# Performance work log

Measured on AMD Instinct MI355X. Metric: run time of the kernel, lower is better.

Reference implementation:

```python
import jax, jax.numpy as jnp
import numpy as np
import math

B, S, D_MODEL, H = 2, 2048, 2048, 16
HD = D_MODEL // H  # head_dim = 128


def setup_inputs() -> dict:
    key = jax.random.key(0)
    ks = jax.random.split(key, 10)
    x = jax.random.normal(ks[0], (B, S, D_MODEL), dtype=jnp.float32)
    # RoPE tables: interleaved-pair layout matching rotate_half (adjacent dims form pairs)
    inv_freq = 1.0 / (10000.0 ** (jnp.arange(0, HD, 2, dtype=jnp.float32) / HD))  # [HD/2]
    angles = jnp.arange(S, dtype=jnp.float32)[:, None] * inv_freq[None, :]        # [S, HD/2]
    angles = jnp.repeat(angles, 2, axis=-1)                                       # [S, HD]
    cos, sin = jnp.cos(angles), jnp.sin(angles)
    # causal mask (1 = keep), broadcastable to [B,H,S,S]
    attn_mask = jnp.tril(jnp.ones((S, S), dtype=bool))[None, None]
    scale = 1.0 / math.sqrt(D_MODEL)
    Wq = jax.random.normal(ks[1], (D_MODEL, D_MODEL), dtype=jnp.float32) * scale
    Wk = jax.random.normal(ks[2], (D_MODEL, D_MODEL), dtype=jnp.float32) * scale
    Wv = jax.random.normal(ks[3], (D_MODEL, D_MODEL), dtype=jnp.float32) * scale
    Wo = jax.random.normal(ks[4], (D_MODEL, D_MODEL), dtype=jnp.float32) * scale
    bq = jnp.zeros((D_MODEL,), jnp.float32)
    bk = jnp.zeros((D_MODEL,), jnp.float32)
    bv = jnp.zeros((D_MODEL,), jnp.float32)
    bo = jnp.zeros((D_MODEL,), jnp.float32)
    return {"x": x, "cos": cos, "sin": sin, "attn_mask": attn_mask,
            "Wq": Wq, "bq": bq, "Wk": Wk, "bk": bk, "Wv": Wv, "bv": bv, "Wo": Wo, "bo": bo}


def _rotate_half(x):
    # pairs adjacent dims: (x0,x1) -> (-x1,x0)
    xr = x.reshape(*x.shape[:-1], -1, 2)
    x1, x2 = xr[..., 0], xr[..., 1]
    return jnp.stack([-x2, x1], axis=-1).reshape(x.shape)


def reference(x, cos, sin, attn_mask, Wq, bq, Wk, bk, Wv, bv, Wo, bo):
    b, s, _ = x.shape
    q = (x @ Wq.T + bq).reshape(b, s, H, HD).transpose(0, 2, 1, 3)  # [B,H,S,HD]
    k = (x @ Wk.T + bk).reshape(b, s, H, HD).transpose(0, 2, 1, 3)
    v = (x @ Wv.T + bv).reshape(b, s, H, HD).transpose(0, 2, 1, 3)
    c = cos[None, None]  # [1,1,S,HD]
    sn = sin[None, None]
    q = q * c + _rotate_half(q) * sn
    k = k * c + _rotate_half(k) * sn
    scores = jnp.einsum('bhqd,bhkd->bhqk', q, k) / math.sqrt(HD)  # [B,H,S,S]
    scores = jnp.where(attn_mask, scores, -jnp.inf)
    attn = jax.nn.softmax(scores, axis=-1)
    out = jnp.einsum('bhqk,bhkd->bhqd', attn, v)  # [B,H,S,HD]
    out = out.transpose(0, 2, 1, 3).reshape(b, s, H * HD)
    return out @ Wo.T + bo
```

## Files before the change

kernel.cpp:

```cpp
#include <hip/hip_runtime.h>
#include <math.h>

typedef __attribute__((ext_vector_type(8))) __bf16 bf16x8;
typedef __attribute__((ext_vector_type(4))) float f32x4;
typedef __attribute__((ext_vector_type(4))) unsigned short us4;
typedef unsigned short u16;
typedef unsigned int u32;

#define DEVI static __device__ __forceinline__

DEVI u16 f2bf(float f) {
  union { float f; unsigned u; } v; v.f = f;
  unsigned r = v.u + 0x7fffu + ((v.u >> 16) & 1u);
  return (u16)(r >> 16);
}

DEVI void async16(const void* g, void* l) {
  __builtin_amdgcn_global_load_lds((const __attribute__((address_space(1))) void*)g,
                                   (__attribute__((address_space(3))) void*)l, 16, 0, 0);
}

DEVI u32 pkbf(float lo, float hi) {
  u32 r;
  asm("v_cvt_pk_bf16_f32 %0, %1, %2" : "=v"(r) : "v"(lo), "v"(hi));
  return r;
}

__global__ __launch_bounds__(256) void cast_bf16(const float* __restrict__ in,
                                                 u16* __restrict__ out, int n) {
  int i = (blockIdx.x * 256 + threadIdx.x) * 4;
  if (i >= n) return;
  float4 v = *(const float4*)(in + i);
  us4 o = { f2bf(v.x), f2bf(v.y), f2bf(v.z), f2bf(v.w) };
  *(us4*)(out + i) = o;
}

template<int MODE>
__global__ __launch_bounds__(256, 2)
void gemm_bt(const u16* __restrict__ A, const u16* __restrict__ B,
             const float* __restrict__ bias,
             const float* __restrict__ cosT, const float* __restrict__ sinT,
             void* __restrict__ outp)
{
  __shared__ __align__(16) u16 As[4096];
  __shared__ __align__(16) u16 Bs[4096];
  const int t = threadIdx.x, w = t >> 6, lane = t & 63;
  const int lrow = lane & 15, lk8 = (lane >> 4) * 8;
  const int brow = blockIdx.y * 128, bcol = blockIdx.x * 128;
  const int wr = (w >> 1) * 64, wc = (w & 1) * 64;

  f32x4 acc[4][4] = {};

  for (int k0 = 0; k0 < 2048; k0 += 32) {
#pragma unroll
    for (int r = 0; r < 2; ++r) {
      int e = (r * 256 + t) * 8;
      async16(A + (size_t)(brow + (e >> 5)) * 2048 + k0 + (e & 31), As + r * 2048 + w * 512);
      async16(B + (size_t)(bcol + (e >> 5)) * 2048 + k0 + (e & 31), Bs + r * 2048 + w * 512);
    }
    __syncthreads();
    bf16x8 a[4], b[4];
#pragma unroll
    for (int m = 0; m < 4; ++m) a[m] = *(const bf16x8*)(As + (wr + m * 16 + lrow) * 32 + lk8);
#pragma unroll
    for (int n = 0; n < 4; ++n) b[n] = *(const bf16x8*)(Bs + (wc + n * 16 + lrow) * 32 + lk8);
#pragma unroll
    for (int m = 0; m < 4; ++m)
#pragma unroll
      for (int n = 0; n < 4; ++n)
        acc[m][n] = __builtin_amdgcn_mfma_f32_16x16x32_bf16(a[m], b[n], acc[m][n], 0, 0, 0);
    __syncthreads();
  }

#pragma unroll
  for (int mi = 0; mi < 4; ++mi) {
#pragma unroll
    for (int ni = 0; ni < 4; ++ni) {
      f32x4 v = acc[mi][ni];
      const int row0 = brow + wr + mi * 16 + (lane >> 4) * 4;
      const int col = bcol + wc + ni * 16 + lrow;
      if constexpr (MODE == 3) {
        float* O = (float*)outp;
        const float bv = bias[col];
#pragma unroll
        for (int r = 0; r < 4; ++r)
          O[(size_t)(row0 + r) * 2048 + col] = v[r] + bv;
      } else if constexpr (MODE == 0 || MODE == 1) {
        u16* O = (u16*)outp;
        const float bv = bias[col];
        const int h = col >> 7, d = col & 127;
        const float sgn = (d & 1) ? 1.f : -1.f;
        const float QSCL = 0.08838834764831845f * 1.44269504088896340f;
#pragma unroll
        for (int r = 0; r < 4; ++r) {
          const int row = row0 + r, bb = row >> 11, s = row & 2047;
          float q = v[r] + bv;
          float p = __shfl_xor(q, 1);
          float o = q * cosT[s * 128 + d] + sgn * p * sinT[s * 128 + d];
          if constexpr (MODE == 0) o *= QSCL;
          u16* base = O + ((size_t)(bb * 16 + h) * 2048 + s) * 128;
          if constexpr (MODE == 0) {
            base[d] = f2bf(o);
          } else {
            *(u16*)((char*)base + (((unsigned)(d << 1)) ^ (unsigned)((s & 7) << 4))) = f2bf(o);
          }
        }
      } else {
        u16* O = (u16*)outp;
        const float bv = bias[col];
        const int h = col >> 7, d = col & 127;
        const int bb = row0 >> 11, s = row0 & 2047;
        us4 ov;
#pragma unroll
        for (int r = 0; r < 4; ++r) ov[r] = f2bf(v[r] + bv);
        const int l = s & 63;
        const int kt = l >> 4, g2 = (l >> 2) & 3;
        const int c = ((kt >> 1) << 5) + (g2 << 3) + ((kt & 1) << 2);
        u16* base = O + ((size_t)(bb * 16 + h) * 128 + d) * 2048 + (s & ~63);
        *(us4*)((char*)base + ((unsigned)(c << 1) ^ (unsigned)((d & 7) << 4))) = ov;
      }
    }
  }
}

__global__ __launch_bounds__(256, 2)
void attn_fwd(const u16* __restrict__ Q, const u16* __restrict__ K,
              const u16* __restrict__ Vt, u16* __restrict__ AO)
{
  __shared__ __align__(16) u16 Ks[2][64 * 128];
  __shared__ __align__(16) u16 Vs[2][128 * 64];
  const int t = threadIdx.x, w = t >> 6, lane = t & 63;
  const int lrow = lane & 15, g = lane >> 4, lk8 = g * 8;
  const int id = blockIdx.x;
  const int bh = (id & 7) | (((id >> 3) & 3) << 3);
  const int pr = id >> 5;
  const u16* Qg = Q + (size_t)bh * 2048 * 128;
  const u16* Kg = K + (size_t)bh * 2048 * 128;
  const u16* Vg = Vt + (size_t)bh * 128 * 2048;
  const int bb = bh >> 4, h = bh & 15;

  for (int half = 0; half < 2; ++half) {
    const int qt = half ? (31 - pr) : pr;
    const int q0 = qt * 64, qw = q0 + w * 16;
    const int nkv = qt + 1;
    const int qg = qw + lrow;

    bf16x8 qf[4];
#pragma unroll
    for (int c = 0; c < 4; ++c)
      qf[c] = *(const bf16x8*)(Qg + (size_t)(qw + lrow) * 128 + lk8 + c * 32);

    f32x4 acc_o[8] = {};
    float m = -1e30f, lsum = 0.f;

    auto stage = [&](int i, int b) {
#pragma unroll
      for (int r = 0; r < 4; ++r) {
        int e = (r * 256 + t) * 8;
        async16(Kg + (size_t)i * 8192 + e, &Ks[b][r * 2048 + w * 512]);
        async16(Vg + (size_t)(e >> 6) * 2048 + i * 64 + (e & 63), &Vs[b][r * 2048 + w * 512]);
      }
    };

    stage(0, 0);
    for (int i = 0; i < nkv; ++i) {
      const int cur = i & 1;
      const bool pfch = (i + 1) < nkv;
      if (pfch) stage(i + 1, cur ^ 1);
      if (pfch) asm volatile("s_waitcnt vmcnt(8)" ::: "memory");
      else      asm volatile("s_waitcnt vmcnt(0)" ::: "memory");
      __builtin_amdgcn_s_barrier();
      __builtin_amdgcn_sched_barrier(0);

      f32x4 sc[4];
      __builtin_amdgcn_s_setprio(1);
#pragma unroll
      for (int kt = 0; kt < 4; ++kt) {
        f32x4 s = {};
        const int krow = kt * 16 + lrow;
        const char* kbase = (const char*)(&Ks[cur][krow * 128]);
        const unsigned sw = (unsigned)((krow & 7) << 4);
#pragma unroll
        for (int c = 0; c < 4; ++c) {
          bf16x8 kf = *(const bf16x8*)(kbase + ((unsigned)((lk8 + c * 32) << 1) ^ sw));
          s = __builtin_amdgcn_mfma_f32_16x16x32_bf16(kf, qf[c], s, 0, 0, 0);
        }
        sc[kt] = s;
      }
      __builtin_amdgcn_s_setprio(0);

      float p[4][4];
      const bool lastblk = (i == qt);
      if (lastblk) {
#pragma unroll
        for (int kt = 0; kt < 4; ++kt)
#pragma unroll
          for (int r = 0; r < 4; ++r) {
            int kg = i * 64 + kt * 16 + g * 4 + r;
            p[kt][r] = (kg > qg) ? -1e30f : sc[kt][r];
          }
      } else {
#pragma unroll
        for (int kt = 0; kt < 4; ++kt)
#pragma unroll
          for (int r = 0; r < 4; ++r) p[kt][r] = sc[kt][r];
      }

      float mm = p[0][0];
#pragma unroll
      for (int kt = 0; kt < 4; ++kt)
#pragma unroll
        for (int r = 0; r < 4; ++r) mm = fmaxf(mm, p[kt][r]);
      mm = fmaxf(mm, __shfl_xor(mm, 16));
      mm = fmaxf(mm, __shfl_xor(mm, 32));

      float rs = 0.f;
      if (__any(mm > m + 8.f)) {
        const float mn = fmaxf(m, mm);
        const float corr = exp2f(m - mn);
        m = mn;
#pragma unroll
        for (int kt = 0; kt < 4; ++kt)
#pragma unroll
          for (int r = 0; r < 4; ++r) { p[kt][r] = exp2f(p[kt][r] - m); rs += p[kt][r]; }
        rs += __shfl_xor(rs, 16);
        rs += __shfl_xor(rs, 32);
        lsum = lsum * corr + rs;
#pragma unroll
        for (int nt = 0; nt < 8; ++nt)
#pragma unroll
          for (int r = 0; r < 4; ++r) acc_o[nt][r] *= corr;
      } else {
#pragma unroll
        for (int kt = 0; kt < 4; ++kt)
#pragma unroll
          for (int r = 0; r < 4; ++r) { p[kt][r] = exp2f(p[kt][r] - m); rs += p[kt][r]; }
        rs += __shfl_xor(rs, 16);
        rs += __shfl_xor(rs, 32);
        lsum += rs;
      }

      bf16x8 pb[2];
#pragma unroll
      for (int kc = 0; kc < 2; ++kc) {
        union { u32 d[4]; bf16x8 v; } u;
        u.d[0] = pkbf(p[2 * kc][0], p[2 * kc][1]);
        u.d[1] = pkbf(p[2 * kc][2], p[2 * kc][3]);
        u.d[2] = pkbf(p[2 * kc + 1][0], p[2 * kc + 1][1]);
        u.d[3] = pkbf(p[2 * kc + 1][2], p[2 * kc + 1][3]);
        pb[kc] = u.v;
      }

      __builtin_amdgcn_s_setprio(1);
#pragma unroll
      for (int nt = 0; nt < 8; ++nt) {
        const int vrow = nt * 16 + lrow;
        const char* vbase = (const char*)(&Vs[cur][vrow * 64]);
        const unsigned sw2 = (unsigned)((vrow & 7) << 4);
#pragma unroll
        for (int kc = 0; kc < 2; ++kc) {
          bf16x8 vf = *(const bf16x8*)(vbase + ((unsigned)((lk8 + kc * 32) << 1) ^ sw2));
          acc_o[nt] = __builtin_amdgcn_mfma_f32_16x16x32_bf16(vf, pb[kc], acc_o[nt], 0, 0, 0);
        }
      }
      __builtin_amdgcn_s_setprio(0);
      __builtin_amdgcn_s_barrier();
    }

    const float inv_l = 1.f / lsum;
#pragma unroll
    for (int nt = 0; nt < 8; ++nt) {
      us4 ov;
#pragma unroll
      for (int r = 0; r < 4; ++r) ov[r] = f2bf(acc_o[nt][r] * inv_l);
      *(us4*)(AO + ((size_t)(bb * 2048 + qg)) * 2048 + h * 128 + nt * 16 + g * 4) = ov;
    }
  }
}

extern "C" void kernel_launch(void* const* d_in, const int* in_sizes, int n_in,
                              void* d_out, int out_size, void* d_ws, size_t ws_size,
                              hipStream_t stream) {
  const float* x    = (const float*)d_in[0];
  const float* cosT = (const float*)d_in[1];
  const float* sinT = (const float*)d_in[2];
  const float* Wq   = (const float*)d_in[4];
  const float* bq   = (const float*)d_in[5];
  const float* Wk   = (const float*)d_in[6];
  const float* bk   = (const float*)d_in[7];
  const float* Wv   = (const float*)d_in[8];
  const float* bv   = (const float*)d_in[9];
  const float* Wo   = (const float*)d_in[10];
  const float* bo   = (const float*)d_in[11];
  float* out = (float*)d_out;

  char* ws = (char*)d_ws;
  u16* xb  = (u16*)(ws);
  u16* Wqb = (u16*)(ws + (16u << 20));
  u16* Wkb = (u16*)(ws + (24u << 20));
  u16* Wvb = (u16*)(ws + (32u << 20));
  u16* Wob = (u16*)(ws + (40u << 20));
  u16* Qb  = (u16*)(ws + (48u << 20));
  u16* Kb  = (u16*)(ws + (64u << 20));
  u16* Vtb = (u16*)(ws + (80u << 20));
  u16* AOb = (u16*)(ws + (96u << 20));

  cast_bf16<<<8192, 256, 0, stream>>>(x,  xb,  4096 * 2048);
  cast_bf16<<<4096, 256, 0, stream>>>(Wq, Wqb, 2048 * 2048);
  cast_bf16<<<4096, 256, 0, stream>>>(Wk, Wkb, 2048 * 2048);
  cast_bf16<<<4096, 256, 0, stream>>>(Wv, Wvb, 2048 * 2048);
  cast_bf16<<<4096, 256, 0, stream>>>(Wo, Wob, 2048 * 2048);

  dim3 gg(16, 32);
  gemm_bt<0><<<gg, 256, 0, stream>>>(xb, Wqb, bq, cosT, sinT, (void*)Qb);
  gemm_bt<1><<<gg, 256, 0, stream>>>(xb, Wkb, bk, cosT, sinT, (void*)Kb);
  gemm_bt<2><<<gg, 256, 0, stream>>>(xb, Wvb, bv, nullptr, nullptr, (void*)Vtb);

  attn_fwd<<<512, 256, 0, stream>>>(Qb, Kb, Vtb, AOb);

  gemm_bt<3><<<gg, 256, 0, stream>>>(AOb, Wob, bo, nullptr, nullptr, (void*)out);
}
```

Before: 289.0 us.

## Replace GEMMs with fused QKV triple-buffered 8-wave 256x128 tile kernel

Replaces the simple single-buffered 128x128 GEMM with a 512-thread, 256x128-tile kernel that uses a 64-wide K step, a triple-buffered LDS ring of async global-to-LDS loads, XOR-swizzled LDS layout and ping-pong MFMA phases with priority hints. The Q, K and V projections are merged into one launch with a combined grid selecting the weight slab per tile. The output projection uses the same kernel. The aim is to hide global memory latency, avoid LDS bank conflicts, cut barrier overhead per MFMA and remove two launches. The cost is more complex synchronisation that relies on hand-written vmcnt waits and about 144KB of LDS per block.

```diff
diff --git a/kernel.cpp b/kernel.cpp
--- a/kernel.cpp
+++ b/kernel.cpp
@@ -35,80 +35,132 @@
   *(us4*)(out + i) = o;
 }
 
-template<int MODE>
-__global__ __launch_bounds__(256, 2)
-void gemm_bt(const u16* __restrict__ A, const u16* __restrict__ B,
-             const float* __restrict__ bias,
-             const float* __restrict__ cosT, const float* __restrict__ sinT,
-             void* __restrict__ outp)
+__global__ __launch_bounds__(512, 2)
+void gemm8p(const u16* __restrict__ A,
+            const u16* __restrict__ W0, const u16* __restrict__ W1, const u16* __restrict__ W2,
+            const float* __restrict__ biasQ, const float* __restrict__ biasK,
+            const float* __restrict__ biasV,
+            const float* __restrict__ cosT, const float* __restrict__ sinT,
+            void* __restrict__ out0, void* __restrict__ out1, void* __restrict__ out2,
+            int ntn, int qkv)
 {
-  __shared__ __align__(16) u16 As[4096];
-  __shared__ __align__(16) u16 Bs[4096];
+  __shared__ __align__(16) char lds[3 * 49152];
   const int t = threadIdx.x, w = t >> 6, lane = t & 63;
-  const int lrow = lane & 15, lk8 = (lane >> 4) * 8;
-  const int brow = blockIdx.y * 128, bcol = blockIdx.x * 128;
-  const int wr = (w >> 1) * 64, wc = (w & 1) * 64;
+  const int lrow = lane & 15, g = lane >> 4, lk8 = g * 8;
+  const int nt = blockIdx.x % ntn, mt = blockIdx.x / ntn;
+  const int slab = qkv ? (nt >> 4) : 3;
+  const u16* Bp = (slab == 1) ? W1 : (slab == 2) ? W2 : W0;
+  const int brow = mt * 256;
+  const int bcol = (qkv ? (nt & 15) : nt) * 128;
+  const int wm = w >> 1, wn = w & 1;
+
+  size_t soff[6];
+#pragma unroll
+  for (int j = 0; j < 6; ++j) {
+    int p = j * 8192 + t * 16;
+    int pr = (j < 4) ? p : (p - 32768);
+    int r = pr >> 7;
+    int c = ((pr ^ ((r & 7) << 4)) & 127) >> 1;
+    soff[j] = (j < 4) ? ((size_t)(brow + r) * 2048 + c)
+                      : ((size_t)(bcol + r) * 2048 + c);
+  }
+  auto stage = [&](int tile, int j, char* buf) {
+    const u16* src = (j < 4) ? A : Bp;
+    async16(src + soff[j] + tile * 64, buf + j * 8192 + t * 16);
+  };
+
+  int offA[4][2], offB[4][2];
+#pragma unroll
+  for (int m = 0; m < 4; ++m)
+#pragma unroll
+    for (int kk = 0; kk < 2; ++kk) {
+      const int c = (lk8 + kk * 32) * 2;
+      const int ra = wm * 64 + m * 16 + lrow;
+      offA[m][kk] = (ra * 128 + c) ^ ((ra & 7) << 4);
+      const int rb = wn * 64 + m * 16 + lrow;
+      offB[m][kk] = 32768 + ((rb * 128 + c) ^ ((rb & 7) << 4));
+    }
 
   f32x4 acc[4][4] = {};
 
-  for (int k0 = 0; k0 < 2048; k0 += 32) {
-#pragma unroll
-    for (int r = 0; r < 2; ++r) {
-      int e = (r * 256 + t) * 8;
-      async16(A + (size_t)(brow + (e >> 5)) * 2048 + k0 + (e & 31), As + r * 2048 + w * 512);
-      async16(B + (size_t)(bcol + (e >> 5)) * 2048 + k0 + (e & 31), Bs + r * 2048 + w * 512);
-    }
-    __syncthreads();
-    bf16x8 a[4], b[4];
-#pragma unroll
-    for (int m = 0; m < 4; ++m) a[m] = *(const bf16x8*)(As + (wr + m * 16 + lrow) * 32 + lk8);
-#pragma unroll
-    for (int n = 0; n < 4; ++n) b[n] = *(const bf16x8*)(Bs + (wc + n * 16 + lrow) * 32 + lk8);
-#pragma unroll
-    for (int m = 0; m < 4; ++m)
+#pragma unroll
+  for (int j = 0; j < 6; ++j) stage(0, j, lds);
+#pragma unroll
+  for (int j = 0; j < 6; ++j) stage(1, j, lds + 49152);
+  asm volatile("s_waitcnt vmcnt(6)" ::: "memory");
+  __builtin_amdgcn_s_barrier();
+
+  for (int tt = 0; tt < 32; ++tt) {
+    char* cur = lds + (tt % 3) * 49152;
+    char* nxt = lds + ((tt + 2) % 3) * 49152;
+    const bool st = (tt + 2) < 32;
+
+    bf16x8 bfr[4][2], afr[2][2];
+#pragma unroll
+    for (int n = 0; n < 4; ++n)
+#pragma unroll
+      for (int kk = 0; kk < 2; ++kk) bfr[n][kk] = *(const bf16x8*)(cur + offB[n][kk]);
+#pragma unroll
+    for (int m = 0; m < 2; ++m)
+#pragma unroll
+      for (int kk = 0; kk < 2; ++kk) afr[m][kk] = *(const bf16x8*)(cur + offA[m][kk]);
+    if (st) { stage(tt + 2, 0, nxt); stage(tt + 2, 1, nxt); stage(tt + 2, 2, nxt); }
+    __builtin_amdgcn_s_barrier();
+    asm volatile("s_waitcnt lgkmcnt(0)" ::: "memory");
+    __builtin_amdgcn_sched_barrier(0);
+    __builtin_amdgcn_s_setprio(1);
+#pragma unroll
+    for (int m = 0; m < 2; ++m)
 #pragma unroll
       for (int n = 0; n < 4; ++n)
-        acc[m][n] = __builtin_amdgcn_mfma_f32_16x16x32_bf16(a[m], b[n], acc[m][n], 0, 0, 0);
-    __syncthreads();
+#pragma unroll
+        for (int kk = 0; kk < 2; ++kk)
+          acc[m][n] = __builtin_amdgcn_mfma_f32_16x16x32_bf16(afr[m][kk], bfr[n][kk], acc[m][n], 0, 0, 0);
+    __builtin_amdgcn_s_setprio(0);
+    __builtin_amdgcn_s_barrier();
+
+#pragma unroll
+    for (int m = 0; m < 2; ++m)
+#pragma unroll
+      for (int kk = 0; kk < 2; ++kk) afr[m][kk] = *(const bf16x8*)(cur + offA[m + 2][kk]);
+    if (st) { stage(tt + 2, 3, nxt); stage(tt + 2, 4, nxt); stage(tt + 2, 5, nxt); }
+    if (tt < 31) {
+      if (st) asm volatile("s_waitcnt vmcnt(6)" ::: "memory");
+      else    asm volatile("s_waitcnt vmcnt(0)" ::: "memory");
+    }
+    __builtin_amdgcn_s_barrier();
+    asm volatile("s_waitcnt lgkmcnt(0)" ::: "memory");
+    __builtin_amdgcn_sched_barrier(0);
+    __builtin_amdgcn_s_setprio(1);
+#pragma unroll
+    for (int m = 0; m < 2; ++m)
+#pragma unroll
+      for (int n = 0; n < 4; ++n)
+#pragma unroll
+        for (int kk = 0; kk < 2; ++kk)
+          acc[m + 2][n] = __builtin_amdgcn_mfma_f32_16x16x32_bf16(afr[m][kk], bfr[n][kk], acc[m + 2][n], 0, 0, 0);
+    __builtin_amdgcn_s_setprio(0);
+    __builtin_amdgcn_s_barrier();
   }
 
+  const int g4 = g * 4;
 #pragma unroll
   for (int mi = 0; mi < 4; ++mi) {
 #pragma unroll
     for (int ni = 0; ni < 4; ++ni) {
       f32x4 v = acc[mi][ni];
-      const int row0 = brow + wr + mi * 16 + (lane >> 4) * 4;
-      const int col = bcol + wc + ni * 16 + lrow;
-      if constexpr (MODE == 3) {
-        float* O = (float*)outp;
-        const float bv = bias[col];
+      const int row0 = brow + wm * 64 + mi * 16 + g4;
+      const int cols = bcol + wn * 64 + ni * 16 + lrow;
+      if (slab == 3) {
+        float* O = (float*)out0;
+        const float bv = biasQ[cols];
 #pragma unroll
         for (int r = 0; r < 4; ++r)
-          O[(size_t)(row0 + r) * 2048 + col] = v[r] + bv;
-      } else if constexpr (MODE == 0 || MODE == 1) {
-        u16* O = (u16*)outp;
-        const float bv = bias[col];
-        const int h = col >> 7, d = col & 127;
-        const float sgn = (d & 1) ? 1.f : -1.f;
-        const float QSCL = 0.08838834764831845f * 1.44269504088896340f;
-#pragma unroll
-        for (int r = 0; r < 4; ++r) {
-          const int row = row0 + r, bb = row >> 11, s = row & 2047;
-          float q = v[r] + bv;
-          float p = __shfl_xor(q, 1);
-          float o = q * cosT[s * 128 + d] + sgn * p * sinT[s * 128 + d];
-          if constexpr (MODE == 0) o *= QSCL;
-          u16* base = O + ((size_t)(bb * 16 + h) * 2048 + s) * 128;
-          if constexpr (MODE == 0) {
-            base[d] = f2bf(o);
-          } else {
-            *(u16*)((char*)base + (((unsigned)(d << 1)) ^ (unsigned)((s & 7) << 4))) = f2bf(o);
-          }
-        }
-      } else {
-        u16* O = (u16*)outp;
-        const float bv = bias[col];
-        const int h = col >> 7, d = col & 127;
+          O[(size_t)(row0 + r) * 2048 + cols] = v[r] + bv;
+      } else if (slab == 2) {
+        u16* O = (u16*)out2;
+        const float bv = biasV[cols];
+        const int h = cols >> 7, d = cols & 127;
         const int bb = row0 >> 11, s = row0 & 2047;
         us4 ov;
 #pragma unroll
@@ -118,6 +170,25 @@
         const int c = ((kt >> 1) << 5) + (g2 << 3) + ((kt & 1) << 2);
         u16* base = O + ((size_t)(bb * 16 + h) * 128 + d) * 2048 + (s & ~63);
         *(us4*)((char*)base + ((unsigned)(c << 1) ^ (unsigned)((d & 7) << 4))) = ov;
+      } else {
+        u16* O = (u16*)(slab ? out1 : out0);
+        const float bv = slab ? biasK[cols] : biasQ[cols];
+        const int h = cols >> 7, d = cols & 127;
+        const float sgn = (d & 1) ? 1.f : -1.f;
+        const float QSCL = 0.08838834764831845f * 1.44269504088896340f;
+#pragma unroll
+        for (int r = 0; r < 4; ++r) {
+          const int row = row0 + r, bb = row >> 11, s = row & 2047;
+          float q = v[r] + bv;
+          float p = __shfl_xor(q, 1);
+          float o = q * cosT[s * 128 + d] + sgn * p * sinT[s * 128 + d];
+          u16* base = O + ((size_t)(bb * 16 + h) * 2048 + s) * 128;
+          if (slab == 0) {
+            base[d] = f2bf(o * QSCL);
+          } else {
+            *(u16*)((char*)base + (((unsigned)(d << 1)) ^ (unsigned)((s & 7) << 4))) = f2bf(o);
+          }
+        }
       }
     }
   }
@@ -311,12 +382,11 @@
   cast_bf16<<<4096, 256, 0, stream>>>(Wv, Wvb, 2048 * 2048);
   cast_bf16<<<4096, 256, 0, stream>>>(Wo, Wob, 2048 * 2048);
 
-  dim3 gg(16, 32);
-  gemm_bt<0><<<gg, 256, 0, stream>>>(xb, Wqb, bq, cosT, sinT, (void*)Qb);
-  gemm_bt<1><<<gg, 256, 0, stream>>>(xb, Wkb, bk, cosT, sinT, (void*)Kb);
-  gemm_bt<2><<<gg, 256, 0, stream>>>(xb, Wvb, bv, nullptr, nullptr, (void*)Vtb);
+  gemm8p<<<768, 512, 0, stream>>>(xb, Wqb, Wkb, Wvb, bq, bk, bv, cosT, sinT,
+                                  (void*)Qb, (void*)Kb, (void*)Vtb, 48, 1);
 
   attn_fwd<<<512, 256, 0, stream>>>(Qb, Kb, Vtb, AOb);
 
-  gemm_bt<3><<<gg, 256, 0, stream>>>(AOb, Wob, bo, nullptr, nullptr, (void*)out);
-}
+  gemm8p<<<256, 512, 0, stream>>>(AOb, Wob, Wob, Wob, bo, bo, bo, nullptr, nullptr,
+                                  (void*)out, nullptr, nullptr, 16, 0);
+}
```

New measurement: 274.7 us. 5.0% less time.

## Merge QKV projections into one launch and double query rows per attention wave

Applied to the files above, without the earlier changes.

The Q, K and V projection GEMMs now run as a single launch with a 48-wide grid, where each block picks its weight slab and epilogue at runtime. The output projection uses the same kernel with the slab forced to the plain fp32 path, and the GEMM launch bound is raised to 4 blocks per CU. The attention kernel now has each wave handle two 16-row query sub-tiles (128 query rows per block), so every K/V tile loaded into LDS is reused twice, and the grid is halved to 256 blocks. The costs are more registers per wave in attention, fewer blocks for load balancing, and runtime branching in the GEMM epilogue.

```diff
diff --git a/kernel.cpp b/kernel.cpp
--- a/kernel.cpp
+++ b/kernel.cpp
@@ -35,18 +35,22 @@
   *(us4*)(out + i) = o;
 }
 
-template<int MODE>
-__global__ __launch_bounds__(256, 2)
-void gemm_bt(const u16* __restrict__ A, const u16* __restrict__ B,
-             const float* __restrict__ bias,
+__global__ __launch_bounds__(256, 4)
+void gemm128(const u16* __restrict__ A,
+             const u16* __restrict__ W0, const u16* __restrict__ W1, const u16* __restrict__ W2,
+             const float* __restrict__ biasQ, const float* __restrict__ biasK,
+             const float* __restrict__ biasV,
              const float* __restrict__ cosT, const float* __restrict__ sinT,
-             void* __restrict__ outp)
+             void* __restrict__ out0, void* __restrict__ out1, void* __restrict__ out2,
+             int qkv)
 {
   __shared__ __align__(16) u16 As[4096];
   __shared__ __align__(16) u16 Bs[4096];
   const int t = threadIdx.x, w = t >> 6, lane = t & 63;
   const int lrow = lane & 15, lk8 = (lane >> 4) * 8;
-  const int brow = blockIdx.y * 128, bcol = blockIdx.x * 128;
+  const int slab = qkv ? (blockIdx.x >> 4) : 3;
+  const u16* Bp = (slab == 1) ? W1 : (slab == 2) ? W2 : W0;
+  const int brow = blockIdx.y * 128, bcol = (blockIdx.x & 15) * 128;
   const int wr = (w >> 1) * 64, wc = (w & 1) * 64;
 
   f32x4 acc[4][4] = {};
@@ -56,7 +60,7 @@
     for (int r = 0; r < 2; ++r) {
       int e = (r * 256 + t) * 8;
       async16(A + (size_t)(brow + (e >> 5)) * 2048 + k0 + (e & 31), As + r * 2048 + w * 512);
-      async16(B + (size_t)(bcol + (e >> 5)) * 2048 + k0 + (e & 31), Bs + r * 2048 + w * 512);
+      async16(Bp + (size_t)(bcol + (e >> 5)) * 2048 + k0 + (e & 31), Bs + r * 2048 + w * 512);
     }
     __syncthreads();
     bf16x8 a[4], b[4];
@@ -78,37 +82,17 @@
     for (int ni = 0; ni < 4; ++ni) {
       f32x4 v = acc[mi][ni];
       const int row0 = brow + wr + mi * 16 + (lane >> 4) * 4;
-      const int col = bcol + wc + ni * 16 + lrow;
-      if constexpr (MODE == 3) {
-        float* O = (float*)outp;
-        const float bv = bias[col];
+      const int cols = bcol + wc + ni * 16 + lrow;
+      if (slab == 3) {
+        float* O = (float*)out0;
+        const float bv = biasQ[cols];
 #pragma unroll
         for (int r = 0; r < 4; ++r)
-          O[(size_t)(row0 + r) * 2048 + col] = v[r] + bv;
-      } else if constexpr (MODE == 0 || MODE == 1) {
-        u16* O = (u16*)outp;
-        const float bv = bias[col];
-        const int h = col >> 7, d = col & 127;
-        const float sgn = (d & 1) ? 1.f : -1.f;
-        const float QSCL = 0.08838834764831845f * 1.44269504088896340f;
-#pragma unroll
-        for (int r = 0; r < 4; ++r) {
-          const int row = row0 + r, bb = row >> 11, s = row & 2047;
-          float q = v[r] + bv;
-          float p = __shfl_xor(q, 1);
-          float o = q * cosT[s * 128 + d] + sgn * p * sinT[s * 128 + d];
-          if constexpr (MODE == 0) o *= QSCL;
-          u16* base = O + ((size_t)(bb * 16 + h) * 2048 + s) * 128;
-          if constexpr (MODE == 0) {
-            base[d] = f2bf(o);
-          } else {
-            *(u16*)((char*)base + (((unsigned)(d << 1)) ^ (unsigned)((s & 7) << 4))) = f2bf(o);
-          }
-        }
-      } else {
-        u16* O = (u16*)outp;
-        const float bv = bias[col];
-        const int h = col >> 7, d = col & 127;
+          O[(size_t)(row0 + r) * 2048 + cols] = v[r] + bv;
+      } else if (slab == 2) {
+        u16* O = (u16*)out2;
+        const float bv = biasV[cols];
+        const int h = cols >> 7, d = cols & 127;
         const int bb = row0 >> 11, s = row0 & 2047;
         us4 ov;
 #pragma unroll
@@ -118,12 +102,31 @@
         const int c = ((kt >> 1) << 5) + (g2 << 3) + ((kt & 1) << 2);
         u16* base = O + ((size_t)(bb * 16 + h) * 128 + d) * 2048 + (s & ~63);
         *(us4*)((char*)base + ((unsigned)(c << 1) ^ (unsigned)((d & 7) << 4))) = ov;
+      } else {
+        u16* O = (u16*)(slab ? out1 : out0);
+        const float bv = slab ? biasK[cols] : biasQ[cols];
+        const int h = cols >> 7, d = cols & 127;
+        const float sgn = (d & 1) ? 1.f : -1.f;
+        const float QSCL = 0.08838834764831845f * 1.44269504088896340f;
+#pragma unroll
+        for (int r = 0; r < 4; ++r) {
+          const int row = row0 + r, bb = row >> 11, s = row & 2047;
+          float q = v[r] + bv;
+          float p = __shfl_xor(q, 1);
+          float o = q * cosT[s * 128 + d] + sgn * p * sinT[s * 128 + d];
+          u16* base = O + ((size_t)(bb * 16 + h) * 2048 + s) * 128;
+          if (slab == 0) {
+            base[d] = f2bf(o * QSCL);
+          } else {
+            *(u16*)((char*)base + (((unsigned)(d << 1)) ^ (unsigned)((s & 7) << 4))) = f2bf(o);
+          }
+        }
       }
     }
   }
 }
 
-__global__ __launch_bounds__(256, 2)
+__global__ __launch_bounds__(256)
 void attn_fwd(const u16* __restrict__ Q, const u16* __restrict__ K,
               const u16* __restrict__ Vt, u16* __restrict__ AO)
 {
@@ -132,35 +135,37 @@
   const int t = threadIdx.x, w = t >> 6, lane = t & 63;
   const int lrow = lane & 15, g = lane >> 4, lk8 = g * 8;
   const int id = blockIdx.x;
-  const int bh = (id & 7) | (((id >> 3) & 3) << 3);
+  const int bh = id & 31;
   const int pr = id >> 5;
   const u16* Qg = Q + (size_t)bh * 2048 * 128;
   const u16* Kg = K + (size_t)bh * 2048 * 128;
   const u16* Vg = Vt + (size_t)bh * 128 * 2048;
   const int bb = bh >> 4, h = bh & 15;
 
+  auto stage = [&](int i, int b) {
+#pragma unroll
+    for (int r = 0; r < 4; ++r) {
+      int e = (r * 256 + t) * 8;
+      async16(Kg + (size_t)i * 8192 + e, &Ks[b][r * 2048 + w * 512]);
+      async16(Vg + (size_t)(e >> 6) * 2048 + i * 64 + (e & 63), &Vs[b][r * 2048 + w * 512]);
+    }
+  };
+
   for (int half = 0; half < 2; ++half) {
-    const int qt = half ? (31 - pr) : pr;
-    const int q0 = qt * 64, qw = q0 + w * 16;
-    const int nkv = qt + 1;
-    const int qg = qw + lrow;
-
-    bf16x8 qf[4];
-#pragma unroll
-    for (int c = 0; c < 4; ++c)
-      qf[c] = *(const bf16x8*)(Qg + (size_t)(qw + lrow) * 128 + lk8 + c * 32);
-
-    f32x4 acc_o[8] = {};
-    float m = -1e30f, lsum = 0.f;
-
-    auto stage = [&](int i, int b) {
-#pragma unroll
-      for (int r = 0; r < 4; ++r) {
-        int e = (r * 256 + t) * 8;
-        async16(Kg + (size_t)i * 8192 + e, &Ks[b][r * 2048 + w * 512]);
-        async16(Vg + (size_t)(e >> 6) * 2048 + i * 64 + (e & 63), &Vs[b][r * 2048 + w * 512]);
-      }
-    };
+    const int qt = half ? (15 - pr) : pr;
+    const int qw = qt * 128 + w * 32;
+    const int nkv = 2 * (qt + 1);
+    const int qg0 = qw + lrow;
+
+    bf16x8 qf[2][4];
+#pragma unroll
+    for (int s2 = 0; s2 < 2; ++s2)
+#pragma unroll
+      for (int c = 0; c < 4; ++c)
+        qf[s2][c] = *(const bf16x8*)(Qg + (size_t)(qw + s2 * 16 + lrow) * 128 + lk8 + c * 32);
+
+    f32x4 acc[2][8] = {};
+    float m[2] = { -1e30f, -1e30f }, lsum[2] = { 0.f, 0.f };
 
     stage(0, 0);
     for (int i = 0; i < nkv; ++i) {
@@ -172,83 +177,88 @@
       __builtin_amdgcn_s_barrier();
       __builtin_amdgcn_sched_barrier(0);
 
-      f32x4 sc[4];
+      f32x4 sc[2][4];
       __builtin_amdgcn_s_setprio(1);
 #pragma unroll
       for (int kt = 0; kt < 4; ++kt) {
-        f32x4 s = {};
+        f32x4 s0 = {}, s1 = {};
         const int krow = kt * 16 + lrow;
         const char* kbase = (const char*)(&Ks[cur][krow * 128]);
         const unsigned sw = (unsigned)((krow & 7) << 4);
 #pragma unroll
         for (int c = 0; c < 4; ++c) {
           bf16x8 kf = *(const bf16x8*)(kbase + ((unsigned)((lk8 + c * 32) << 1) ^ sw));
-          s = __builtin_amdgcn_mfma_f32_16x16x32_bf16(kf, qf[c], s, 0, 0, 0);
-        }
-        sc[kt] = s;
+          s0 = __builtin_amdgcn_mfma_f32_16x16x32_bf16(kf, qf[0][c], s0, 0, 0, 0);
+          s1 = __builtin_amdgcn_mfma_f32_16x16x32_bf16(kf, qf[1][c], s1, 0, 0, 0);
+        }
+        sc[0][kt] = s0; sc[1][kt] = s1;
       }
       __builtin_amdgcn_s_setprio(0);
 
-      float p[4][4];
-      const bool lastblk = (i == qt);
-      if (lastblk) {
+      const bool guard = (i * 64 + 63) > qw;
+      bf16x8 pb[2][2];
+#pragma unroll
+      for (int s2 = 0; s2 < 2; ++s2) {
+        const int qgs = qg0 + s2 * 16;
+        float p[4][4];
+        if (guard) {
+#pragma unroll
+          for (int kt = 0; kt < 4; ++kt)
+#pragma unroll
+            for (int r = 0; r < 4; ++r) {
+              int kg = i * 64 + kt * 16 + g * 4 + r;
+              p[kt][r] = (kg > qgs) ? -1e30f : sc[s2][kt][r];
+            }
+        } else {
+#pragma unroll
+          for (int kt = 0; kt < 4; ++kt)
+#pragma unroll
+            for (int r = 0; r < 4; ++r) p[kt][r] = sc[s2][kt][r];
+        }
+
+        float mm = p[0][0];
 #pragma unroll
         for (int kt = 0; kt < 4; ++kt)
 #pragma unroll
-          for (int r = 0; r < 4; ++r) {
-            int kg = i * 64 + kt * 16 + g * 4 + r;
-            p[kt][r] = (kg > qg) ? -1e30f : sc[kt][r];
-          }
-      } else {
-#pragma unroll
-        for (int kt = 0; kt < 4; ++kt)
-#pragma unroll
-          for (int r = 0; r < 4; ++r) p[kt][r] = sc[kt][r];
-      }
-
-      float mm = p[0][0];
-#pragma unroll
-      for (int kt = 0; kt < 4; ++kt)
-#pragma unroll
-        for (int r = 0; r < 4; ++r) mm = fmaxf(mm, p[kt][r]);
-      mm = fmaxf(mm, __shfl_xor(mm, 16));
-      mm = fmaxf(mm, __shfl_xor(mm, 32));
-
-      float rs = 0.f;
-      if (__any(mm > m + 8.f)) {
-        const float mn = fmaxf(m, mm);
-        const float corr = exp2f(m - mn);
-        m = mn;
-#pragma unroll
-        for (int kt = 0; kt < 4; ++kt)
-#pragma unroll
-          for (int r = 0; r < 4; ++r) { p[kt][r] = exp2f(p[kt][r] - m); rs += p[kt][r]; }
-        rs += __shfl_xor(rs, 16);
-        rs += __shfl_xor(rs, 32);
-        lsum = lsum * corr + rs;
-#pragma unroll
-        for (int nt = 0; nt < 8; ++nt)
-#pragma unroll
-          for (int r = 0; r < 4; ++r) acc_o[nt][r] *= corr;
-      } else {
-#pragma unroll
-        for (int kt = 0; kt < 4; ++kt)
-#pragma unroll
-          for (int r = 0; r < 4; ++r) { p[kt][r] = exp2f(p[kt][r] - m); rs += p[kt][r]; }
-        rs += __shfl_xor(rs, 16);
-        rs += __shfl_xor(rs, 32);
-        lsum += rs;
-      }
-
-      bf16x8 pb[2];
-#pragma unroll
-      for (int kc = 0; kc < 2; ++kc) {
-        union { u32 d[4]; bf16x8 v; } u;
-        u.d[0] = pkbf(p[2 * kc][0], p[2 * kc][1]);
-        u.d[1] = pkbf(p[2 * kc][2], p[2 * kc][3]);
-        u.d[2] = pkbf(p[2 * kc + 1][0], p[2 * kc + 1][1]);
-        u.d[3] = pkbf(p[2 * kc + 1][2], p[2 * kc + 1][3]);
-        pb[kc] = u.v;
+          for (int r = 0; r < 4; ++r) mm = fmaxf(mm, p[kt][r]);
+        mm = fmaxf(mm, __shfl_xor(mm, 16));
+        mm = fmaxf(mm, __shfl_xor(mm, 32));
+
+        float rs = 0.f;
+        if (__any(mm > m[s2] + 8.f)) {
+          const float mn = fmaxf(m[s2], mm);
+          const float corr = exp2f(m[s2] - mn);
+          m[s2] = mn;
+#pragma unroll
+          for (int kt = 0; kt < 4; ++kt)
+#pragma unroll
+            for (int r = 0; r < 4; ++r) { p[kt][r] = exp2f(p[kt][r] - m[s2]); rs += p[kt][r]; }
+          rs += __shfl_xor(rs, 16);
+          rs += __shfl_xor(rs, 32);
+          lsum[s2] = lsum[s2] * corr + rs;
+#pragma unroll
+          for (int nt = 0; nt < 8; ++nt)
+#pragma unroll
+            for (int r = 0; r < 4; ++r) acc[s2][nt][r] *= corr;
+        } else {
+#pragma unroll
+          for (int kt = 0; kt < 4; ++kt)
+#pragma unroll
+            for (int r = 0; r < 4; ++r) { p[kt][r] = exp2f(p[kt][r] - m[s2]); rs += p[kt][r]; }
+          rs += __shfl_xor(rs, 16);
+          rs += __shfl_xor(rs, 32);
+          lsum[s2] += rs;
+        }
+
+#pragma unroll
+        for (int kc = 0; kc < 2; ++kc) {
+          union { u32 d[4]; bf16x8 v; } u;
+          u.d[0] = pkbf(p[2 * kc][0], p[2 * kc][1]);
+          u.d[1] = pkbf(p[2 * kc][2], p[2 * kc][3]);
+          u.d[2] = pkbf(p[2 * kc + 1][0], p[2 * kc + 1][1]);
+          u.d[3] = pkbf(p[2 * kc + 1][2], p[2 * kc + 1][3]);
+          pb[s2][kc] = u.v;
+        }
       }
 
       __builtin_amdgcn_s_setprio(1);
@@ -260,20 +270,25 @@
 #pragma unroll
         for (int kc = 0; kc < 2; ++kc) {
           bf16x8 vf = *(const bf16x8*)(vbase + ((unsigned)((lk8 + kc * 32) << 1) ^ sw2));
-          acc_o[nt] = __builtin_amdgcn_mfma_f32_16x16x32_bf16(vf, pb[kc], acc_o[nt], 0, 0, 0);
+          acc[0][nt] = __builtin_amdgcn_mfma_f32_16x16x32_bf16(vf, pb[0][kc], acc[0][nt], 0, 0, 0);
+          acc[1][nt] = __builtin_amdgcn_mfma_f32_16x16x32_bf16(vf, pb[1][kc], acc[1][nt], 0, 0, 0);
         }
       }
       __builtin_amdgcn_s_setprio(0);
       __builtin_amdgcn_s_barrier();
     }
 
-    const float inv_l = 1.f / lsum;
-#pragma unroll
-    for (int nt = 0; nt < 8; ++nt) {
-      us4 ov;
-#pragma unroll
-      for (int r = 0; r < 4; ++r) ov[r] = f2bf(acc_o[nt][r] * inv_l);
-      *(us4*)(AO + ((size_t)(bb * 2048 + qg)) * 2048 + h * 128 + nt * 16 + g * 4) = ov;
+#pragma unroll
+    for (int s2 = 0; s2 < 2; ++s2) {
+      const float inv_l = 1.f / lsum[s2];
+      const int qgs = qg0 + s2 * 16;
+#pragma unroll
+      for (int nt = 0; nt < 8; ++nt) {
+        us4 ov;
+#pragma unroll
+        for (int r = 0; r < 4; ++r) ov[r] = f2bf(acc[s2][nt][r] * inv_l);
+        *(us4*)(AO + ((size_t)(bb * 2048 + qgs)) * 2048 + h * 128 + nt * 16 + g * 4) = ov;
+      }
     }
   }
 }
@@ -311,12 +326,13 @@
   cast_bf16<<<4096, 256, 0, stream>>>(Wv, Wvb, 2048 * 2048);
   cast_bf16<<<4096, 256, 0, stream>>>(Wo, Wob, 2048 * 2048);
 
-  dim3 gg(16, 32);
-  gemm_bt<0><<<gg, 256, 0, stream>>>(xb, Wqb, bq, cosT, sinT, (void*)Qb);
-  gemm_bt<1><<<gg, 256, 0, stream>>>(xb, Wkb, bk, cosT, sinT, (void*)Kb);
-  gemm_bt<2><<<gg, 256, 0, stream>>>(xb, Wvb, bv, nullptr, nullptr, (void*)Vtb);
-
-  attn_fwd<<<512, 256, 0, stream>>>(Qb, Kb, Vtb, AOb);
-
-  gemm_bt<3><<<gg, 256, 0, stream>>>(AOb, Wob, bo, nullptr, nullptr, (void*)out);
-}
+  gemm128<<<dim3(48, 32), 256, 0, stream>>>(xb, Wqb, Wkb, Wvb, bq, bk, bv,
+                                            cosT, sinT,
+                                            (void*)Qb, (void*)Kb, (void*)Vtb, 1);
+
+  attn_fwd<<<256, 256, 0, stream>>>(Qb, Kb, Vtb, AOb);
+
+  gemm128<<<dim3(16, 32), 256, 0, stream>>>(AOb, Wob, Wob, Wob, bo, bo, bo,
+                                            nullptr, nullptr,
+                                            (void*)out, nullptr, nullptr, 0);
+}
```

After: 318.9 us. +10.3%, slower.

## Double GEMM K-tile with XOR-swizzled LDS and merge cast kernels

Applied to the files above, without the earlier changes.

The GEMM now stages a 64-wide K slice per iteration instead of 32. The LDS layout uses an XOR swizzle on 16-byte chunks to avoid bank conflicts, and global/LDS offsets are precomputed outside the loop. This halves the number of barrier pairs per GEMM and should cut LDS bank conflicts. The occupancy hint is raised to 3 blocks per CU even though LDS use doubles to 32KB per block. The five separate fp32-to-bf16 cast launches are merged into one kernel to save launch overhead.

```diff
diff --git a/kernel.cpp b/kernel.cpp
--- a/kernel.cpp
+++ b/kernel.cpp
@@ -26,49 +26,83 @@
   return r;
 }
 
-__global__ __launch_bounds__(256) void cast_bf16(const float* __restrict__ in,
-                                                 u16* __restrict__ out, int n) {
+__global__ __launch_bounds__(256)
+void cast_all(const float* __restrict__ x,
+              const float* __restrict__ wq, const float* __restrict__ wk,
+              const float* __restrict__ wv, const float* __restrict__ wo,
+              u16* __restrict__ xb, u16* __restrict__ wqb, u16* __restrict__ wkb,
+              u16* __restrict__ wvb, u16* __restrict__ wob)
+{
+  const int NX = 4096 * 2048, NW = 2048 * 2048;
   int i = (blockIdx.x * 256 + threadIdx.x) * 4;
-  if (i >= n) return;
-  float4 v = *(const float4*)(in + i);
+  const float* src; u16* dst; int off;
+  if (i < NX)               { src = x;  dst = xb;  off = i; }
+  else if (i < NX + NW)     { src = wq; dst = wqb; off = i - NX; }
+  else if (i < NX + 2 * NW) { src = wk; dst = wkb; off = i - NX - NW; }
+  else if (i < NX + 3 * NW) { src = wv; dst = wvb; off = i - NX - 2 * NW; }
+  else                      { src = wo; dst = wob; off = i - NX - 3 * NW; }
+  float4 v = *(const float4*)(src + off);
   us4 o = { f2bf(v.x), f2bf(v.y), f2bf(v.z), f2bf(v.w) };
-  *(us4*)(out + i) = o;
+  *(us4*)(dst + off) = o;
 }
 
 template<int MODE>
-__global__ __launch_bounds__(256, 2)
+__global__ __launch_bounds__(256, 3)
 void gemm_bt(const u16* __restrict__ A, const u16* __restrict__ B,
              const float* __restrict__ bias,
              const float* __restrict__ cosT, const float* __restrict__ sinT,
              void* __restrict__ outp)
 {
-  __shared__ __align__(16) u16 As[4096];
-  __shared__ __align__(16) u16 Bs[4096];
+  __shared__ __align__(16) u16 As[8192];
+  __shared__ __align__(16) u16 Bs[8192];
   const int t = threadIdx.x, w = t >> 6, lane = t & 63;
   const int lrow = lane & 15, lk8 = (lane >> 4) * 8;
   const int brow = blockIdx.y * 128, bcol = blockIdx.x * 128;
   const int wr = (w >> 1) * 64, wc = (w & 1) * 64;
 
+  u32 sA[4], sB[4];
+#pragma unroll
+  for (int r = 0; r < 4; ++r) {
+    const int q = (r * 256 + t) * 16;
+    const int row = q >> 7;
+    const int cb = (q ^ ((row & 7) << 4)) & 127;
+    sA[r] = (u32)((brow + row) * 2048 + (cb >> 1));
+    sB[r] = (u32)((bcol + row) * 2048 + (cb >> 1));
+  }
+
+  int offA[4][2], offB[4][2];
+#pragma unroll
+  for (int m = 0; m < 4; ++m)
+#pragma unroll
+    for (int kk = 0; kk < 2; ++kk) {
+      int row = wr + m * 16 + lrow;
+      offA[m][kk] = (row * 128 + (kk * 32 + lk8) * 2) ^ ((row & 7) << 4);
+      row = wc + m * 16 + lrow;
+      offB[m][kk] = (row * 128 + (kk * 32 + lk8) * 2) ^ ((row & 7) << 4);
+    }
+
   f32x4 acc[4][4] = {};
 
-  for (int k0 = 0; k0 < 2048; k0 += 32) {
-#pragma unroll
-    for (int r = 0; r < 2; ++r) {
-      int e = (r * 256 + t) * 8;
-      async16(A + (size_t)(brow + (e >> 5)) * 2048 + k0 + (e & 31), As + r * 2048 + w * 512);
-      async16(B + (size_t)(bcol + (e >> 5)) * 2048 + k0 + (e & 31), Bs + r * 2048 + w * 512);
+  for (int k0 = 0; k0 < 2048; k0 += 64) {
+#pragma unroll
+    for (int r = 0; r < 4; ++r) {
+      async16(A + sA[r] + k0, (char*)As + (r * 256 + t) * 16);
+      async16(B + sB[r] + k0, (char*)Bs + (r * 256 + t) * 16);
     }
     __syncthreads();
-    bf16x8 a[4], b[4];
-#pragma unroll
-    for (int m = 0; m < 4; ++m) a[m] = *(const bf16x8*)(As + (wr + m * 16 + lrow) * 32 + lk8);
-#pragma unroll
-    for (int n = 0; n < 4; ++n) b[n] = *(const bf16x8*)(Bs + (wc + n * 16 + lrow) * 32 + lk8);
-#pragma unroll
-    for (int m = 0; m < 4; ++m)
-#pragma unroll
-      for (int n = 0; n < 4; ++n)
-        acc[m][n] = __builtin_amdgcn_mfma_f32_16x16x32_bf16(a[m], b[n], acc[m][n], 0, 0, 0);
+#pragma unroll
+    for (int kk = 0; kk < 2; ++kk) {
+      bf16x8 a[4], b[4];
+#pragma unroll
+      for (int m = 0; m < 4; ++m) a[m] = *(const bf16x8*)((char*)As + offA[m][kk]);
+#pragma unroll
+      for (int n = 0; n < 4; ++n) b[n] = *(const bf16x8*)((char*)Bs + offB[n][kk]);
+#pragma unroll
+      for (int m = 0; m < 4; ++m)
+#pragma unroll
+        for (int n = 0; n < 4; ++n)
+          acc[m][n] = __builtin_amdgcn_mfma_f32_16x16x32_bf16(a[m], b[n], acc[m][n], 0, 0, 0);
+    }
     __syncthreads();
   }
 
@@ -305,11 +339,7 @@
   u16* Vtb = (u16*)(ws + (80u << 20));
   u16* AOb = (u16*)(ws + (96u << 20));
 
-  cast_bf16<<<8192, 256, 0, stream>>>(x,  xb,  4096 * 2048);
-  cast_bf16<<<4096, 256, 0, stream>>>(Wq, Wqb, 2048 * 2048);
-  cast_bf16<<<4096, 256, 0, stream>>>(Wk, Wkb, 2048 * 2048);
-  cast_bf16<<<4096, 256, 0, stream>>>(Wv, Wvb, 2048 * 2048);
-  cast_bf16<<<4096, 256, 0, stream>>>(Wo, Wob, 2048 * 2048);
+  cast_all<<<24576, 256, 0, stream>>>(x, Wq, Wk, Wv, Wo, xb, Wqb, Wkb, Wvb, Wob);
 
   dim3 gg(16, 32);
   gemm_bt<0><<<gg, 256, 0, stream>>>(xb, Wqb, bq, cosT, sinT, (void*)Qb);
```

After: 247.2 us, median of 2. -14.5%, faster.
